# Kernel optimization log

Hardware: AMD Instinct MI355X
Metric: run time of the kernel (lower is better)

Reference implementation:

```python
import jax, jax.numpy as jnp
import numpy as np

D_MODEL = 1024
N_SEQ = 2048
H = 16


def _rope_tables(d, n_seq):
    # theta_i = 10000^(-2i/d), i in [0, d/2)
    i = jnp.arange(d // 2, dtype=jnp.float32)
    theta = jnp.power(10000.0, -2.0 * i / d)                 # [d/2]
    ang = jnp.arange(n_seq, dtype=jnp.float32)[:, None] * theta[None, :]  # [S, d/2]
    cos = jnp.repeat(jnp.cos(ang), 2, axis=-1)               # [S, d] (cos duplicated per pair)
    s = jnp.sin(ang)
    sin = jnp.stack([s, -s], axis=-1).reshape(n_seq, d)      # [S, d] (+sin, -sin interleaved)
    return cos, sin


def _apply_rope(x, cos, sin):
    d = x.shape[-1]
    # swap adjacent pairs: (x0,x1,x2,x3,...) -> (x1,x0,x3,x2,...)
    x2 = x.reshape(x.shape[:-1] + (d // 2, 2))[..., ::-1].reshape(x.shape)
    return x * cos + x2 * sin


def setup_inputs() -> dict:
    key = jax.random.key(0)
    ks = jax.random.split(key, 8)
    B, S, D = 2, N_SEQ, D_MODEL
    scale = 1.0 / np.sqrt(D)
    return {
        "q": jax.random.normal(ks[0], (B, S, D), dtype=jnp.float32),
        "k": jax.random.normal(ks[1], (B, S, D), dtype=jnp.float32),
        "v": jax.random.normal(ks[2], (B, S, D), dtype=jnp.float32),
        "W_q": jax.random.normal(ks[3], (D, D), dtype=jnp.float32) * scale,
        "W_k": jax.random.normal(ks[4], (D, D), dtype=jnp.float32) * scale,
        "W_v": jax.random.normal(ks[5], (D, D), dtype=jnp.float32) * scale,
        "W_o": jax.random.normal(ks[6], (D, D), dtype=jnp.float32) * scale,
        "b_o": jax.random.normal(ks[7], (D,), dtype=jnp.float32) * scale,
    }


def reference(q, k, v, W_q, W_k, W_v, W_o, b_o):
    B, S, D = q.shape
    d_k = D // H
    cos, sin = _rope_tables(D, N_SEQ)

    query = _apply_rope(q @ W_q.T, cos, sin)  # RoPE over full d_model, pre head-split
    key_ = _apply_rope(k @ W_k.T, cos, sin)
    value = v @ W_v.T

    def split_heads(x):
        return x.reshape(B, S, H, d_k).transpose(0, 2, 1, 3)  # [B,H,S,dk]

    qh, kh, vh = split_heads(query), split_heads(key_), split_heads(value)

    scores = jnp.einsum("bhsd,bhtd->bhst", qh, kh) / jnp.sqrt(jnp.float32(d_k))
    attn = jax.nn.softmax(scores, axis=-1)
    y = jnp.einsum("bhst,bhtd->bhsd", attn, vh)               # [B,H,S,dk]
    y = y.transpose(0, 2, 1, 3).reshape(B, S, D)
    return y @ W_o.T + b_o
```

## Files before the change

kernel.cpp:

```cpp
#include <hip/hip_runtime.h>
#include <hip/hip_bf16.h>

using bf16 = __hip_bfloat16;
using bf16x8 = __attribute__((ext_vector_type(8))) short;
using f32x4 = __attribute__((ext_vector_type(4))) float;

#define LOG2E 1.44269504088896f

__device__ __forceinline__ void gload_lds16(const void* g, void* lds) {
    __builtin_amdgcn_global_load_lds(
        (const __attribute__((address_space(1))) void*)g,
        (__attribute__((address_space(3))) void*)lds, 16, 0, 0);
}

struct __align__(16) BH8 { bf16 h[8]; };
struct __align__(8)  BH4 { bf16 h[4]; };

struct CvtArgs { const float* src[7]; BH8* dst[7]; };

__global__ __launch_bounds__(256) void cvt_rope(CvtArgs ca,
        float* __restrict__ ct, float* __restrict__ st) {
    int bid = blockIdx.x;
    if (bid < 8192) {
        int i = bid * 256 + threadIdx.x;
        const float* src; BH8* dst; int off;
        if (i < 3 * 524288) {
            int w = i >> 19; off = i & 524287;
            src = ca.src[w]; dst = ca.dst[w];
        } else {
            int j = i - 3 * 524288;
            int w = 3 + (j >> 17); off = j & 131071;
            src = ca.src[w]; dst = ca.dst[w];
        }
        const float4* p = (const float4*)src + (size_t)off * 2;
        float4 a = p[0], b = p[1];
        BH8 r;
        r.h[0] = __float2bfloat16(a.x); r.h[1] = __float2bfloat16(a.y);
        r.h[2] = __float2bfloat16(a.z); r.h[3] = __float2bfloat16(a.w);
        r.h[4] = __float2bfloat16(b.x); r.h[5] = __float2bfloat16(b.y);
        r.h[6] = __float2bfloat16(b.z); r.h[7] = __float2bfloat16(b.w);
        dst[off] = r;
    } else {
        int idx = (bid - 8192) * 256 + threadIdx.x;
        if (idx >= 2048 * 512) return;
        int s = idx >> 9, i = idx & 511;
        float theta = exp2f((float)i * -0.0259525632413075f);
        float ang = (float)s * theta;
        ct[idx] = cosf(ang);
        st[idx] = sinf(ang);
    }
}

struct ProjArgs {
    const bf16* A[3];
    const bf16* W[3];
    void* out[3];
    int mode[3];
};

template <int MF>
__global__ __launch_bounds__(256, 2) void gemm_bt(ProjArgs pa,
        const float* __restrict__ ct, const float* __restrict__ st,
        const float* __restrict__ bias) {
    constexpr int Kd = 1024;
    constexpr int BM = MF * 32;
    __shared__ __align__(16) bf16 As[BM * 32];
    __shared__ __align__(16) bf16 Bs[128 * 32];
    const int z = blockIdx.z;
    const bf16* __restrict__ A = pa.A[z];
    const bf16* __restrict__ W = pa.W[z];
    const int mode = pa.mode[z];
    const int tid = threadIdx.x, wid = tid >> 6, lane = tid & 63;
    const int g = lane >> 4, l15 = lane & 15;
    const int wm = wid >> 1, wn = wid & 1;
    const int m0 = blockIdx.y * BM, n0 = blockIdx.x * 128;
    f32x4 acc[MF][4] = {};
    const int sbyte = wid * 1024 + lane * 16;

    for (int kb = 0; kb < Kd; kb += 32) {
        __syncthreads();
#pragma unroll
        for (int r = 0; r < MF / 2; ++r) {
            int byte = sbyte + r * 4096;
            int row = byte >> 6, cb = byte & 63;
            int csrc = cb ^ (((row >> 1) & 3) << 4);
            gload_lds16((const char*)(A + (size_t)(m0 + row) * Kd + kb) + csrc,
                        (char*)As + wid * 1024 + r * 4096);
        }
#pragma unroll
        for (int r = 0; r < 2; ++r) {
            int byte = sbyte + r * 4096;
            int row = byte >> 6, cb = byte & 63;
            int csrc = cb ^ (((row >> 1) & 3) << 4);
            gload_lds16((const char*)(W + (size_t)(n0 + row) * Kd + kb) + csrc,
                        (char*)Bs + wid * 1024 + r * 4096);
        }
        __syncthreads();
        bf16x8 af[MF], bw[4];
#pragma unroll
        for (int i = 0; i < MF; ++i) {
            int ra = wm * (MF * 16) + i * 16 + l15;
            af[i] = *(const bf16x8*)((const char*)As + ra * 64 +
                                     ((g * 16) ^ (((ra >> 1) & 3) << 4)));
        }
#pragma unroll
        for (int j = 0; j < 4; ++j) {
            int rb = wn * 64 + j * 16 + l15;
            bw[j] = *(const bf16x8*)((const char*)Bs + rb * 64 +
                                     ((g * 16) ^ (((rb >> 1) & 3) << 4)));
        }
#pragma unroll
        for (int i = 0; i < MF; ++i)
#pragma unroll
            for (int j = 0; j < 4; ++j)
                acc[i][j] = __builtin_amdgcn_mfma_f32_16x16x32_bf16(af[i], bw[j], acc[i][j], 0, 0, 0);
    }

    if (mode == 0) {
        float* out = (float*)pa.out[z];
#pragma unroll
        for (int i = 0; i < MF; ++i) {
            int row = m0 + wm * (MF * 16) + i * 16 + g * 4;
#pragma unroll
            for (int j = 0; j < 4; ++j) {
                int col = n0 + wn * 64 + j * 16 + l15;
                float bv = bias[col];
#pragma unroll
                for (int r = 0; r < 4; ++r)
                    out[(size_t)(row + r) * 1024 + col] = acc[i][j][r] + bv;
            }
        }
    } else if (mode == 3) {
        bf16* out = (bf16*)pa.out[z];
#pragma unroll
        for (int i = 0; i < MF; ++i) {
            int m = m0 + wm * (MF * 16) + i * 16 + g * 4;
            int b = m >> 11, s = m & 2047;
#pragma unroll
            for (int j = 0; j < 4; ++j) {
                int col = n0 + wn * 64 + j * 16 + l15;
                int h = col >> 6, dv = col & 63;
                BH4 pk;
#pragma unroll
                for (int r = 0; r < 4; ++r) pk.h[r] = __float2bfloat16(acc[i][j][r]);
                *(BH4*)(out + (((size_t)(b * 16 + h)) * 64 + dv) * 2048 + s) = pk;
            }
        }
    } else {
        bf16* out = (bf16*)pa.out[z];
        float scl = (mode == 1) ? (0.125f * LOG2E) : 1.0f;
#pragma unroll
        for (int i = 0; i < MF; ++i) {
            int mrow = m0 + wm * (MF * 16) + i * 16 + g * 4;
#pragma unroll
            for (int j = 0; j < 4; ++j) {
                int col = n0 + wn * 64 + j * 16 + l15;
                int ci = col >> 1;
                float sgn = (col & 1) ? -1.0f : 1.0f;
                int h = col >> 6, dv = col & 63;
#pragma unroll
                for (int r = 0; r < 4; ++r) {
                    int m = mrow + r;
                    int b = m >> 11, s = m & 2047;
                    float vv = acc[i][j][r];
                    float pv = __shfl_xor(vv, 1);
                    float c = ct[s * 512 + ci], sn = st[s * 512 + ci];
                    float o = (vv * c + sgn * sn * pv) * scl;
                    out[(((size_t)(b * 16 + h)) * 2048 + s) * 64 + dv] = __float2bfloat16(o);
                }
            }
        }
    }
}

__global__ __launch_bounds__(64, 2) void attn_fwd(
        const bf16* __restrict__ Qh, const bf16* __restrict__ Kh,
        const bf16* __restrict__ Vt, bf16* __restrict__ Y) {
    __shared__ __align__(16) bf16 Ks[2][64 * 64];
    const int lane = threadIdx.x & 63;
    const int g = lane >> 4, l15 = lane & 15;
    const int lin = blockIdx.x;
    const int swz = (lin & 7) * 256 + (lin >> 3);
    const int bh = swz >> 6, qt = swz & 63;
    const int q0 = qt * 32;
    const bf16* Qb = Qh + (size_t)bh * 2048 * 64;
    const bf16* Kb = Kh + (size_t)bh * 2048 * 64;
    const bf16* Vb = Vt + (size_t)bh * 64 * 2048;

    bf16x8 aq[2][2];
#pragma unroll
    for (int qfr = 0; qfr < 2; ++qfr)
#pragma unroll
        for (int kk = 0; kk < 2; ++kk)
            aq[qfr][kk] = *(const bf16x8*)(Qb + (size_t)(q0 + qfr * 16 + l15) * 64 + kk * 32 + g * 8);

    f32x4 yacc[2][4] = {};
    float lrow[2] = {0.f, 0.f};

    int csrc[8], kph[8];
#pragma unroll
    for (int i = 0; i < 8; ++i) {
        int byte = lane * 16 + i * 1024;
        int L = byte >> 7;
        csrc[i] = (byte & 127) ^ ((L & 7) << 4);
        kph[i] = ((L >> 5) << 5) + (((L >> 2) & 3) << 3) + (((L >> 4) & 1) << 2) + (L & 3);
    }

#define STAGE(T, BUF)                                                          \
    do {                                                                       \
        _Pragma("unroll")                                                      \
        for (int i = 0; i < 8; ++i)                                            \
            gload_lds16((const char*)(Kb + (size_t)((T) * 64 + kph[i]) * 64) + csrc[i], \
                        (char*)&Ks[BUF][0] + i * 1024);                        \
    } while (0)

    STAGE(0, 0);

    for (int t = 0; t < 32; ++t) {
        bf16x8 vf[4][2];
#pragma unroll
        for (int dn = 0; dn < 4; ++dn)
#pragma unroll
            for (int ch = 0; ch < 2; ++ch)
                vf[dn][ch] = *(const bf16x8*)(Vb + (size_t)(dn * 16 + l15) * 2048 +
                                              t * 64 + ch * 32 + g * 8);
        if (t < 31) {
            STAGE(t + 1, (t + 1) & 1);
            asm volatile("s_waitcnt vmcnt(16)" ::: "memory");
        } else {
            asm volatile("s_waitcnt vmcnt(8)" ::: "memory");
        }
        const char* Kst = (const char*)&Ks[t & 1][0];

        f32x4 sacc[4][2] = {};
#pragma unroll
        for (int kk = 0; kk < 2; ++kk) {
            bf16x8 kf[4];
#pragma unroll
            for (int kfr = 0; kfr < 4; ++kfr)
                kf[kfr] = *(const bf16x8*)(Kst + (kfr * 16 + l15) * 128 +
                                           ((kk * 64 + g * 16) ^ ((l15 & 7) << 4)));
#pragma unroll
            for (int kfr = 0; kfr < 4; ++kfr)
#pragma unroll
                for (int qfr = 0; qfr < 2; ++qfr)
                    sacc[kfr][qfr] = __builtin_amdgcn_mfma_f32_16x16x32_bf16(
                        kf[kfr], aq[qfr][kk], sacc[kfr][qfr], 0, 0, 0);
        }

        bf16x8 ap[2][2];
#pragma unroll
        for (int qfr = 0; qfr < 2; ++qfr)
#pragma unroll
            for (int ch = 0; ch < 2; ++ch) {
                bf16 hh[8];
#pragma unroll
                for (int r = 0; r < 4; ++r) {
                    float x = exp2f(sacc[2 * ch][qfr][r]);
                    lrow[qfr] += x;
                    hh[r] = __float2bfloat16(x);
                }
#pragma unroll
                for (int r = 0; r < 4; ++r) {
                    float x = exp2f(sacc[2 * ch + 1][qfr][r]);
                    lrow[qfr] += x;
                    hh[4 + r] = __float2bfloat16(x);
                }
                ap[qfr][ch] = *(const bf16x8*)hh;
            }

#pragma unroll
        for (int ch = 0; ch < 2; ++ch)
#pragma unroll
            for (int qfr = 0; qfr < 2; ++qfr)
#pragma unroll
                for (int dn = 0; dn < 4; ++dn)
                    yacc[qfr][dn] = __builtin_amdgcn_mfma_f32_16x16x32_bf16(
                        ap[qfr][ch], vf[dn][ch], yacc[qfr][dn], 0, 0, 0);
    }
#undef STAGE

    const int b = bh >> 4, h = bh & 15;
#pragma unroll
    for (int qfr = 0; qfr < 2; ++qfr) {
        float ls = lrow[qfr];
        ls += __shfl_xor(ls, 16);
        ls += __shfl_xor(ls, 32);
#pragma unroll
        for (int r = 0; r < 4; ++r) {
            float lv = __shfl(ls, g * 4 + r);
            float inv = 1.0f / lv;
            int s = q0 + qfr * 16 + g * 4 + r;
            bf16* yp = Y + ((size_t)(b * 2048 + s)) * 1024 + h * 64;
#pragma unroll
            for (int dn = 0; dn < 4; ++dn)
                yp[dn * 16 + l15] = __float2bfloat16(yacc[qfr][dn][r] * inv);
        }
    }
}

extern "C" void kernel_launch(void* const* d_in, const int* in_sizes, int n_in,
                              void* d_out, int out_size, void* d_ws, size_t ws_size,
                              hipStream_t stream) {
    const float* q  = (const float*)d_in[0];
    const float* k  = (const float*)d_in[1];
    const float* v  = (const float*)d_in[2];
    const float* Wq = (const float*)d_in[3];
    const float* Wk = (const float*)d_in[4];
    const float* Wv = (const float*)d_in[5];
    const float* Wo = (const float*)d_in[6];
    const float* bo = (const float*)d_in[7];

    const size_t MB = 1048576ull;
    if (ws_size < 72 * MB) return;
    char* p = (char*)d_ws;
    bf16* qb  = (bf16*)(p + 0 * MB);
    bf16* kb  = (bf16*)(p + 8 * MB);
    bf16* vb  = (bf16*)(p + 16 * MB);
    bf16* Wqb = (bf16*)(p + 24 * MB);
    bf16* Wkb = (bf16*)(p + 26 * MB);
    bf16* Wvb = (bf16*)(p + 28 * MB);
    bf16* Wob = (bf16*)(p + 30 * MB);
    bf16* Qh  = (bf16*)(p + 32 * MB);
    bf16* Kh  = (bf16*)(p + 40 * MB);
    bf16* Vt  = (bf16*)(p + 48 * MB);
    bf16* Yb  = (bf16*)(p + 56 * MB);
    float* ct = (float*)(p + 64 * MB);
    float* st = (float*)(p + 68 * MB);

    CvtArgs ca;
    ca.src[0] = q;  ca.dst[0] = (BH8*)qb;
    ca.src[1] = k;  ca.dst[1] = (BH8*)kb;
    ca.src[2] = v;  ca.dst[2] = (BH8*)vb;
    ca.src[3] = Wq; ca.dst[3] = (BH8*)Wqb;
    ca.src[4] = Wk; ca.dst[4] = (BH8*)Wkb;
    ca.src[5] = Wv; ca.dst[5] = (BH8*)Wvb;
    ca.src[6] = Wo; ca.dst[6] = (BH8*)Wob;
    cvt_rope<<<12288, 256, 0, stream>>>(ca, ct, st);

    ProjArgs pa;
    pa.A[0] = qb;  pa.A[1] = kb;  pa.A[2] = vb;
    pa.W[0] = Wqb; pa.W[1] = Wkb; pa.W[2] = Wvb;
    pa.out[0] = Qh; pa.out[1] = Kh; pa.out[2] = Vt;
    pa.mode[0] = 1; pa.mode[1] = 2; pa.mode[2] = 3;
    gemm_bt<4><<<dim3(8, 32, 3), 256, 0, stream>>>(pa, ct, st, nullptr);

    attn_fwd<<<2048, 64, 0, stream>>>(Qh, Kh, Vt, Yb);

    ProjArgs pf;
    pf.A[0] = Yb; pf.A[1] = Yb; pf.A[2] = Yb;
    pf.W[0] = Wob; pf.W[1] = Wob; pf.W[2] = Wob;
    pf.out[0] = d_out; pf.out[1] = d_out; pf.out[2] = d_out;
    pf.mode[0] = 0; pf.mode[1] = 0; pf.mode[2] = 0;
    gemm_bt<2><<<dim3(8, 64, 1), 256, 0, stream>>>(pf, ct, st, bo);
}
```

Measured before the change: 169.8 us.

## Split attention over key halves with shared-K two-wave blocks and a combine pass

The attention kernel now splits the key range into two halves processed by separate blocks. Each 128-thread block runs two waves that cover 64 query rows and cooperatively stage a shared K tile in LDS, synchronised with __syncthreads. Each half writes unnormalised fp32 partial outputs and row sums to workspace, and a new combine kernel adds the halves, normalises and writes bf16 Y. The aim is more wave-level parallelism and less redundant K traffic per query row, at the cost of an extra kernel launch, fp32 partial-result traffic and reuse of workspace regions that overlap earlier buffers.

```diff
diff --git a/kernel.cpp b/kernel.cpp
--- a/kernel.cpp
+++ b/kernel.cpp
@@ -173,16 +173,20 @@
     }
 }
 
-__global__ __launch_bounds__(64, 2) void attn_fwd(
+__global__ __launch_bounds__(128, 4) void attn_fwd(
         const bf16* __restrict__ Qh, const bf16* __restrict__ Kh,
-        const bf16* __restrict__ Vt, bf16* __restrict__ Y) {
+        const bf16* __restrict__ Vt, float* __restrict__ PO,
+        float* __restrict__ PL) {
     __shared__ __align__(16) bf16 Ks[2][64 * 64];
-    const int lane = threadIdx.x & 63;
+    const int tid = threadIdx.x, wid = tid >> 6, lane = tid & 63;
     const int g = lane >> 4, l15 = lane & 15;
     const int lin = blockIdx.x;
     const int swz = (lin & 7) * 256 + (lin >> 3);
-    const int bh = swz >> 6, qt = swz & 63;
-    const int q0 = qt * 32;
+    const int bh = swz >> 6;
+    const int qt = (swz >> 1) & 31;
+    const int half = swz & 1;
+    const int q0 = qt * 64 + wid * 32;
+    const int t0 = half * 16;
     const bf16* Qb = Qh + (size_t)bh * 2048 * 64;
     const bf16* Kb = Kh + (size_t)bh * 2048 * 64;
     const bf16* Vb = Vt + (size_t)bh * 64 * 2048;
@@ -197,10 +201,10 @@
     f32x4 yacc[2][4] = {};
     float lrow[2] = {0.f, 0.f};
 
-    int csrc[8], kph[8];
-#pragma unroll
-    for (int i = 0; i < 8; ++i) {
-        int byte = lane * 16 + i * 1024;
+    int csrc[4], kph[4];
+#pragma unroll
+    for (int i = 0; i < 4; ++i) {
+        int byte = tid * 16 + i * 2048;
         int L = byte >> 7;
         csrc[i] = (byte & 127) ^ ((L & 7) << 4);
         kph[i] = ((L >> 5) << 5) + (((L >> 2) & 3) << 3) + (((L >> 4) & 1) << 2) + (L & 3);
@@ -209,14 +213,18 @@
 #define STAGE(T, BUF)                                                          \
     do {                                                                       \
         _Pragma("unroll")                                                      \
-        for (int i = 0; i < 8; ++i)                                            \
+        for (int i = 0; i < 4; ++i)                                            \
             gload_lds16((const char*)(Kb + (size_t)((T) * 64 + kph[i]) * 64) + csrc[i], \
-                        (char*)&Ks[BUF][0] + i * 1024);                        \
+                        (char*)&Ks[BUF][0] + tid * 16 + i * 2048);             \
     } while (0)
 
-    STAGE(0, 0);
-
-    for (int t = 0; t < 32; ++t) {
+    STAGE(t0, 0);
+
+    for (int tt = 0; tt < 16; ++tt) {
+        const int t = t0 + tt;
+        __syncthreads();
+        if (tt < 15) STAGE(t + 1, (tt + 1) & 1);
+
         bf16x8 vf[4][2];
 #pragma unroll
         for (int dn = 0; dn < 4; ++dn)
@@ -224,13 +232,8 @@
             for (int ch = 0; ch < 2; ++ch)
                 vf[dn][ch] = *(const bf16x8*)(Vb + (size_t)(dn * 16 + l15) * 2048 +
                                               t * 64 + ch * 32 + g * 8);
-        if (t < 31) {
-            STAGE(t + 1, (t + 1) & 1);
-            asm volatile("s_waitcnt vmcnt(16)" ::: "memory");
-        } else {
-            asm volatile("s_waitcnt vmcnt(8)" ::: "memory");
-        }
-        const char* Kst = (const char*)&Ks[t & 1][0];
+
+        const char* Kst = (const char*)&Ks[tt & 1][0];
 
         f32x4 sacc[4][2] = {};
 #pragma unroll
@@ -280,23 +283,48 @@
     }
 #undef STAGE
 
-    const int b = bh >> 4, h = bh & 15;
+    float* POb = PO + ((size_t)(half * 32 + bh)) * 2048 * 64;
+    float* PLb = PL + ((size_t)(half * 32 + bh)) * 2048;
 #pragma unroll
     for (int qfr = 0; qfr < 2; ++qfr) {
         float ls = lrow[qfr];
         ls += __shfl_xor(ls, 16);
         ls += __shfl_xor(ls, 32);
+        if (g == 0) PLb[q0 + qfr * 16 + l15] = ls;
 #pragma unroll
         for (int r = 0; r < 4; ++r) {
-            float lv = __shfl(ls, g * 4 + r);
-            float inv = 1.0f / lv;
             int s = q0 + qfr * 16 + g * 4 + r;
-            bf16* yp = Y + ((size_t)(b * 2048 + s)) * 1024 + h * 64;
 #pragma unroll
             for (int dn = 0; dn < 4; ++dn)
-                yp[dn * 16 + l15] = __float2bfloat16(yacc[qfr][dn][r] * inv);
-        }
-    }
+                POb[(size_t)s * 64 + dn * 16 + l15] = yacc[qfr][dn][r];
+        }
+    }
+}
+
+__global__ __launch_bounds__(256) void attn_combine(
+        const float* __restrict__ PO, const float* __restrict__ PL,
+        bf16* __restrict__ Y) {
+    int i = blockIdx.x * 256 + threadIdx.x;
+    int gidx = i & 7;
+    int s = (i >> 3) & 2047;
+    int bh = i >> 14;
+    size_t o = ((size_t)bh * 2048 + s) * 64 + gidx * 8;
+    const float4* a0 = (const float4*)(PO + o);
+    const float4* a1 = (const float4*)(PO + 4194304ull + o);
+    float l = PL[bh * 2048 + s] + PL[65536 + bh * 2048 + s];
+    float inv = 1.0f / l;
+    float4 x0 = a0[0], x1 = a0[1], y0 = a1[0], y1 = a1[1];
+    int b = bh >> 4, h = bh & 15;
+    BH8 r;
+    r.h[0] = __float2bfloat16((x0.x + y0.x) * inv);
+    r.h[1] = __float2bfloat16((x0.y + y0.y) * inv);
+    r.h[2] = __float2bfloat16((x0.z + y0.z) * inv);
+    r.h[3] = __float2bfloat16((x0.w + y0.w) * inv);
+    r.h[4] = __float2bfloat16((x1.x + y1.x) * inv);
+    r.h[5] = __float2bfloat16((x1.y + y1.y) * inv);
+    r.h[6] = __float2bfloat16((x1.z + y1.z) * inv);
+    r.h[7] = __float2bfloat16((x1.w + y1.w) * inv);
+    *(BH8*)(Y + ((size_t)(b * 2048 + s)) * 1024 + h * 64 + gidx * 8) = r;
 }
 
 extern "C" void kernel_launch(void* const* d_in, const int* in_sizes, int n_in,
@@ -320,11 +348,13 @@
     bf16* Wqb = (bf16*)(p + 24 * MB);
     bf16* Wkb = (bf16*)(p + 26 * MB);
     bf16* Wvb = (bf16*)(p + 28 * MB);
-    bf16* Wob = (bf16*)(p + 30 * MB);
-    bf16* Qh  = (bf16*)(p + 32 * MB);
-    bf16* Kh  = (bf16*)(p + 40 * MB);
-    bf16* Vt  = (bf16*)(p + 48 * MB);
-    bf16* Yb  = (bf16*)(p + 56 * MB);
+    bf16* Wob = (bf16*)(p + 38 * MB);
+    bf16* Qh  = (bf16*)(p + 40 * MB);
+    bf16* Kh  = (bf16*)(p + 48 * MB);
+    bf16* Vt  = (bf16*)(p + 56 * MB);
+    float* PO = (float*)(p + 0 * MB);
+    float* PL = (float*)(p + 32 * MB);
+    bf16* Yb  = (bf16*)(p + 40 * MB);
     float* ct = (float*)(p + 64 * MB);
     float* st = (float*)(p + 68 * MB);
 
@@ -345,7 +375,8 @@
     pa.mode[0] = 1; pa.mode[1] = 2; pa.mode[2] = 3;
     gemm_bt<4><<<dim3(8, 32, 3), 256, 0, stream>>>(pa, ct, st, nullptr);
 
-    attn_fwd<<<2048, 64, 0, stream>>>(Qh, Kh, Vt, Yb);
+    attn_fwd<<<2048, 128, 0, stream>>>(Qh, Kh, Vt, PO, PL);
+    attn_combine<<<2048, 256, 0, stream>>>(PO, PL, Yb);
 
     ProjArgs pf;
     pf.A[0] = Yb; pf.A[1] = Yb; pf.A[2] = Yb;
```

Result: slower. 182.3 us, median of 2 (+7.4%).
